# Kernel tuning notes

Hardware: AMD Instinct MI355X
Metric: run time of the kernel (lower is better)

Reference implementation:

```python
import jax, jax.numpy as jnp
import numpy as np

TEMPERATURE = 0.07
ALPHA = 1.0
GAMMA = 2.0
EPS = 1e-12  # F.normalize eps


def _l2_normalize(x):
    # matches F.normalize: x / max(||x||_2, eps)
    norm = jnp.sqrt(jnp.sum(x * x, axis=-1, keepdims=True))
    return x / jnp.maximum(norm, EPS)


def setup_inputs() -> dict:
    key = jax.random.key(0)
    k1, k2 = jax.random.split(key)
    B, D = 8192, 64
    image_features = jax.random.normal(k1, (B, D), dtype=jnp.float32)
    text_features = jax.random.normal(k2, (B, D), dtype=jnp.float32)
    return {"image_features": image_features, "text_features": text_features}


def reference(image_features, text_features):
    img = _l2_normalize(image_features)
    txt = _l2_normalize(text_features)
    logits = jnp.einsum("bd,cd->bc", img, txt) / TEMPERATURE  # [B, B]
    B = logits.shape[0]
    idx = jnp.arange(B)

    logp_row = jax.nn.log_softmax(logits, axis=-1)  # i2t CE source
    logp_col = jax.nn.log_softmax(logits, axis=0)   # t2i CE source

    diag_logp_row = logp_row[idx, idx]
    diag_logp_col = logp_col[idx, idx]

    # focal weight uses ROW-softmax positive prob for BOTH directions (as in source)
    p_pos = jnp.exp(diag_logp_row)
    w = ALPHA * (1.0 - p_pos) ** GAMMA

    focal_i2t = jnp.mean(w * (-diag_logp_row))
    focal_t2i = jnp.mean(w * (-diag_logp_col))
    return (focal_i2t + focal_t2i) / 2.0
```

## Files before the change

### kernel.cpp

```cpp
#include <hip/hip_runtime.h>
#include <hip/hip_bf16.h>


#define NB 8192
#define ND 64

constexpr float INV_T = 1.0f / 0.07f;
constexpr float LOG2E = 1.4426950408889634f;
constexpr float LN2   = 0.6931471805599453f;
constexpr float K1    = INV_T * LOG2E;

typedef float  floatx4 __attribute__((ext_vector_type(4)));
typedef short  bf16x8  __attribute__((ext_vector_type(8)));

__global__ __launch_bounds__(256)
void norm_kernel(const float* __restrict__ img, const float* __restrict__ txt,
                 __hip_bfloat16* __restrict__ imgB,
                 __hip_bfloat16* __restrict__ txtB,
                 float* __restrict__ diag,
                 float* __restrict__ out)
{
    if (blockIdx.x == 0 && threadIdx.x == 0) out[0] = 0.f;
    const int lane = threadIdx.x & 63;
    const int row  = blockIdx.x * 4 + (threadIdx.x >> 6);
    const float x = img[row * ND + lane];
    const float t = txt[row * ND + lane];
    float sx = x * x, st = t * t, sxt = x * t;
    #pragma unroll
    for (int o = 1; o < 64; o <<= 1) {
        sx  += __shfl_xor(sx,  o, 64);
        st  += __shfl_xor(st,  o, 64);
        sxt += __shfl_xor(sxt, o, 64);
    }
    const float nx_den = fmaxf(sqrtf(sx), 1e-12f);
    const float nt_den = fmaxf(sqrtf(st), 1e-12f);
    imgB[row * ND + lane] = __float2bfloat16(x / nx_den * K1);
    txtB[row * ND + lane] = __float2bfloat16(t / nt_den);
    if (lane == 0) diag[row] = sxt / (nx_den * nt_den) * INV_T;
}

__global__ __launch_bounds__(256)
void score_kernel(const __hip_bfloat16* __restrict__ imgB,
                  const __hip_bfloat16* __restrict__ txtB,
                  float* __restrict__ rowPart,
                  float* __restrict__ colPart)
{
    const int wid   = threadIdx.x >> 6;
    const int lane  = threadIdx.x & 63;
    const int gw    = blockIdx.x * 4 + wid;
    const int strip = gw >> 5;
    const int chunk = gw & 31;
    const int m = lane & 15;
    const int q = lane >> 4;

    const bf16x8* __restrict__ A  = (const bf16x8*)imgB;
    const bf16x8* __restrict__ Bp = (const bf16x8*)txtB;

    const int rowbase = strip * 64;
    bf16x8 a[4][2];
    #pragma unroll
    for (int it = 0; it < 4; ++it) {
        const int r = rowbase + it * 16 + m;
        a[it][0] = A[r * 8 + q];
        a[it][1] = A[r * 8 + 4 + q];
    }

    const int colbase = chunk * 256 + m;
    bf16x8 b0 = Bp[colbase * 8 + q];
    bf16x8 b1 = Bp[colbase * 8 + 4 + q];

    float rs[16];
    #pragma unroll
    for (int i = 0; i < 16; ++i) rs[i] = 0.f;

    const floatx4 NEGK = {-K1, -K1, -K1, -K1};

    #pragma unroll 2
    for (int t = 0; t < 16; ++t) {
        const int nn = colbase + (((t + 1) & 15) << 4);
        const bf16x8 pb0 = Bp[nn * 8 + q];
        const bf16x8 pb1 = Bp[nn * 8 + 4 + q];

        float csp[4];
        #pragma unroll
        for (int it = 0; it < 4; ++it) {
            floatx4 z   = __builtin_amdgcn_mfma_f32_16x16x32_bf16(a[it][0], b0, NEGK, 0, 0, 0);
            floatx4 acc = __builtin_amdgcn_mfma_f32_16x16x32_bf16(a[it][1], b1, z,    0, 0, 0);
            const float e0 = __builtin_amdgcn_exp2f(acc[0]);
            const float e1 = __builtin_amdgcn_exp2f(acc[1]);
            const float e2 = __builtin_amdgcn_exp2f(acc[2]);
            const float e3 = __builtin_amdgcn_exp2f(acc[3]);
            rs[it * 4 + 0] += e0;
            rs[it * 4 + 1] += e1;
            rs[it * 4 + 2] += e2;
            rs[it * 4 + 3] += e3;
            csp[it] = (e0 + e1) + (e2 + e3);
        }
        float cs = (csp[0] + csp[1]) + (csp[2] + csp[3]);
        cs += __shfl_xor(cs, 16, 64);
        cs += __shfl_xor(cs, 32, 64);
        if (q == 0) colPart[strip * NB + colbase + (t << 4)] = cs;
        b0 = pb0; b1 = pb1;
    }

    #pragma unroll
    for (int idx = 0; idx < 16; ++idx) {
        float v = rs[idx];
        v += __shfl_xor(v, 1, 64);
        v += __shfl_xor(v, 2, 64);
        v += __shfl_xor(v, 4, 64);
        v += __shfl_xor(v, 8, 64);
        if (m == idx) {
            const int it = idx >> 2, r = idx & 3;
            rowPart[chunk * NB + rowbase + it * 16 + q * 4 + r] = v;
        }
    }
}

__global__ __launch_bounds__(256)
void finish_kernel(const float* __restrict__ rowPart,
                   const float* __restrict__ colPart,
                   const float* __restrict__ diag,
                   float* __restrict__ out)
{
    const int i = blockIdx.x * 256 + threadIdx.x;
    float rowS = 0.f, colS = 0.f;
    #pragma unroll 4
    for (int c = 0; c < 32; ++c)  rowS += rowPart[c * NB + i];
    #pragma unroll 4
    for (int s = 0; s < 128; ++s) colS += colPart[s * NB + i];
    const float d     = diag[i];
    const float lse_r = INV_T + __builtin_amdgcn_logf(rowS) * LN2;
    const float lse_c = INV_T + __builtin_amdgcn_logf(colS) * LN2;
    const float lpr = d - lse_r;
    const float lpc = d - lse_c;
    const float p   = __builtin_amdgcn_exp2f(lpr * LOG2E);
    const float om  = 1.f - p;
    float contrib = om * om * (-lpr - lpc) * (0.5f / (float)NB);

    #pragma unroll
    for (int o = 1; o < 64; o <<= 1) contrib += __shfl_xor(contrib, o, 64);
    __shared__ float red[4];
    if ((threadIdx.x & 63) == 0) red[threadIdx.x >> 6] = contrib;
    __syncthreads();
    if (threadIdx.x == 0)
        atomicAdd(out, red[0] + red[1] + red[2] + red[3]);
}

extern "C" void kernel_launch(void* const* d_in, const int* in_sizes, int n_in,
                              void* d_out, int out_size, void* d_ws, size_t ws_size,
                              hipStream_t stream)
{
    const float* img = (const float*)d_in[0];
    const float* txt = (const float*)d_in[1];

    char* ws = (char*)d_ws;
    __hip_bfloat16* imgB = (__hip_bfloat16*)(ws);
    __hip_bfloat16* txtB = (__hip_bfloat16*)(ws + (1u << 20));
    float* diag    = (float*)(ws + (2u << 20));
    float* rowPart = (float*)(ws + (2u << 20) + (1u << 16));
    float* colPart = (float*)(ws + (3u << 20) + (1u << 16));

    norm_kernel<<<NB / 4, 256, 0, stream>>>(img, txt, imgB, txtB, diag, (float*)d_out);
    score_kernel<<<1024, 256, 0, stream>>>(imgB, txtB, rowPart, colPart);
    finish_kernel<<<NB / 256, 256, 0, stream>>>(rowPart, colPart, diag, (float*)d_out);
}
```

Baseline: 97.42 us.

## Replace partial-sum buffers with atomic row/col accumulation and vectorize normalization

```diff
diff --git a/kernel.cpp b/kernel.cpp
--- a/kernel.cpp
+++ b/kernel.cpp
@@ -12,38 +12,58 @@
 
 typedef float  floatx4 __attribute__((ext_vector_type(4)));
 typedef short  bf16x8  __attribute__((ext_vector_type(8)));
+typedef short  shortx4 __attribute__((ext_vector_type(4)));
 
 __global__ __launch_bounds__(256)
 void norm_kernel(const float* __restrict__ img, const float* __restrict__ txt,
                  __hip_bfloat16* __restrict__ imgB,
                  __hip_bfloat16* __restrict__ txtB,
                  float* __restrict__ diag,
+                 float* __restrict__ rowSum,
+                 float* __restrict__ colSum,
                  float* __restrict__ out)
 {
-    if (blockIdx.x == 0 && threadIdx.x == 0) out[0] = 0.f;
+    const int tid = blockIdx.x * 256 + threadIdx.x;
+    if (tid < NB) { rowSum[tid] = 0.f; colSum[tid] = 0.f; }
+    if (tid == 0) out[0] = 0.f;
+
     const int lane = threadIdx.x & 63;
-    const int row  = blockIdx.x * 4 + (threadIdx.x >> 6);
-    const float x = img[row * ND + lane];
-    const float t = txt[row * ND + lane];
-    float sx = x * x, st = t * t, sxt = x * t;
+    const int gw   = blockIdx.x * 4 + (threadIdx.x >> 6);
+    const int sub  = lane >> 4;
+    const int c16  = lane & 15;
+    const int row  = gw * 4 + sub;
+
+    const floatx4 x = ((const floatx4*)img)[row * 16 + c16];
+    const floatx4 t = ((const floatx4*)txt)[row * 16 + c16];
+    float sx  = x[0]*x[0] + x[1]*x[1] + x[2]*x[2] + x[3]*x[3];
+    float st  = t[0]*t[0] + t[1]*t[1] + t[2]*t[2] + t[3]*t[3];
+    float sxt = x[0]*t[0] + x[1]*t[1] + x[2]*t[2] + x[3]*t[3];
     #pragma unroll
-    for (int o = 1; o < 64; o <<= 1) {
+    for (int o = 1; o < 16; o <<= 1) {
         sx  += __shfl_xor(sx,  o, 64);
         st  += __shfl_xor(st,  o, 64);
         sxt += __shfl_xor(sxt, o, 64);
     }
-    const float nx_den = fmaxf(sqrtf(sx), 1e-12f);
-    const float nt_den = fmaxf(sqrtf(st), 1e-12f);
-    imgB[row * ND + lane] = __float2bfloat16(x / nx_den * K1);
-    txtB[row * ND + lane] = __float2bfloat16(t / nt_den);
-    if (lane == 0) diag[row] = sxt / (nx_den * nt_den) * INV_T;
+    const float nx = fmaxf(sqrtf(sx), 1e-12f);
+    const float nt = fmaxf(sqrtf(st), 1e-12f);
+    shortx4 xb, tb;
+    #pragma unroll
+    for (int j = 0; j < 4; ++j) {
+        __hip_bfloat16 hx = __float2bfloat16(x[j] / nx * K1);
+        __hip_bfloat16 ht = __float2bfloat16(t[j] / nt);
+        xb[j] = *reinterpret_cast<const short*>(&hx);
+        tb[j] = *reinterpret_cast<const short*>(&ht);
+    }
+    ((shortx4*)imgB)[row * 16 + c16] = xb;
+    ((shortx4*)txtB)[row * 16 + c16] = tb;
+    if (c16 == 0) diag[row] = sxt / (nx * nt) * INV_T;
 }
 
 __global__ __launch_bounds__(256)
 void score_kernel(const __hip_bfloat16* __restrict__ imgB,
                   const __hip_bfloat16* __restrict__ txtB,
-                  float* __restrict__ rowPart,
-                  float* __restrict__ colPart)
+                  float* __restrict__ rowSum,
+                  float* __restrict__ colSum)
 {
     const int wid   = threadIdx.x >> 6;
     const int lane  = threadIdx.x & 63;
@@ -99,36 +119,41 @@
         float cs = (csp[0] + csp[1]) + (csp[2] + csp[3]);
         cs += __shfl_xor(cs, 16, 64);
         cs += __shfl_xor(cs, 32, 64);
-        if (q == 0) colPart[strip * NB + colbase + (t << 4)] = cs;
+        if (q == 0)
+            unsafeAtomicAdd(&colSum[colbase + (t << 4)], cs);
         b0 = pb0; b1 = pb1;
     }
 
-    #pragma unroll
-    for (int idx = 0; idx < 16; ++idx) {
-        float v = rs[idx];
-        v += __shfl_xor(v, 1, 64);
-        v += __shfl_xor(v, 2, 64);
-        v += __shfl_xor(v, 4, 64);
-        v += __shfl_xor(v, 8, 64);
-        if (m == idx) {
-            const int it = idx >> 2, r = idx & 3;
-            rowPart[chunk * NB + rowbase + it * 16 + q * 4 + r] = v;
-        }
+#define RS_STAGE(d)                                                     \
+    {                                                                   \
+        const bool hi = (m & (d)) != 0;                                 \
+        _Pragma("unroll")                                               \
+        for (int j = 0; j < (d); ++j) {                                 \
+            const float va = rs[j], vb = rs[j + (d)];                   \
+            const float send = hi ? va : vb;                            \
+            const float recv = __shfl_xor(send, (d), 64);               \
+            rs[j] = (hi ? vb : va) + recv;                              \
+        }                                                               \
     }
+    RS_STAGE(8)
+    RS_STAGE(4)
+    RS_STAGE(2)
+    RS_STAGE(1)
+#undef RS_STAGE
+
+    const int row = rowbase + ((m >> 2) << 4) + (q << 2) + (m & 3);
+    unsafeAtomicAdd(&rowSum[row], rs[0]);
 }
 
 __global__ __launch_bounds__(256)
-void finish_kernel(const float* __restrict__ rowPart,
-                   const float* __restrict__ colPart,
+void finish_kernel(const float* __restrict__ rowSum,
+                   const float* __restrict__ colSum,
                    const float* __restrict__ diag,
                    float* __restrict__ out)
 {
     const int i = blockIdx.x * 256 + threadIdx.x;
-    float rowS = 0.f, colS = 0.f;
-    #pragma unroll 4
-    for (int c = 0; c < 32; ++c)  rowS += rowPart[c * NB + i];
-    #pragma unroll 4
-    for (int s = 0; s < 128; ++s) colS += colPart[s * NB + i];
+    const float rowS = rowSum[i];
+    const float colS = colSum[i];
     const float d     = diag[i];
     const float lse_r = INV_T + __builtin_amdgcn_logf(rowS) * LN2;
     const float lse_c = INV_T + __builtin_amdgcn_logf(colS) * LN2;
@@ -157,11 +182,11 @@
     char* ws = (char*)d_ws;
     __hip_bfloat16* imgB = (__hip_bfloat16*)(ws);
     __hip_bfloat16* txtB = (__hip_bfloat16*)(ws + (1u << 20));
-    float* diag    = (float*)(ws + (2u << 20));
-    float* rowPart = (float*)(ws + (2u << 20) + (1u << 16));
-    float* colPart = (float*)(ws + (3u << 20) + (1u << 16));
+    float* diag   = (float*)(ws + (2u << 20));
+    float* rowSum = (float*)(ws + (2u << 20) + (1u << 15));
+    float* colSum = (float*)(ws + (2u << 20) + (2u << 15));
 
-    norm_kernel<<<NB / 4, 256, 0, stream>>>(img, txt, imgB, txtB, diag, (float*)d_out);
-    score_kernel<<<1024, 256, 0, stream>>>(imgB, txtB, rowPart, colPart);
-    finish_kernel<<<NB / 256, 256, 0, stream>>>(rowPart, colPart, diag, (float*)d_out);
+    norm_kernel<<<512, 256, 0, stream>>>(img, txt, imgB, txtB, diag, rowSum, colSum, (float*)d_out);
+    score_kernel<<<1024, 256, 0, stream>>>(imgB, txtB, rowSum, colSum);
+    finish_kernel<<<NB / 256, 256, 0, stream>>>(rowSum, colSum, diag, (float*)d_out);
 }
```

New measurement: 83.15 us. -14.7%, faster.
